# Performance work log

Hardware: AMD Instinct MI355X
Metric: run time of the kernel (lower is better)

## Reference

```python
import math
import jax, jax.numpy as jnp
import numpy as np

D_MODEL = 4096
N_HEADS = 32
N_KV_HEADS = 8
D_HEAD = D_MODEL // N_HEADS  # 128
GROUP = N_HEADS // N_KV_HEADS  # 4
ROPE = dict(rope_theta=500000.0, factor=32.0, hi_freq_factor=4.0, lo_freq_factor=1.0, original_context_length=8192)


def setup_inputs() -> dict:
    key = jax.random.key(0)
    ks = jax.random.split(key, 5)
    B, T = 1, 2048
    s = 0.02
    return {
        "resid": jax.random.normal(ks[0], (B, T, D_MODEL), jnp.float32),
        "Wq": jax.random.normal(ks[1], (D_MODEL, D_MODEL), jnp.float32) * s,
        "Wk": jax.random.normal(ks[2], (D_MODEL, N_KV_HEADS * D_HEAD), jnp.float32) * s,
        "Wv": jax.random.normal(ks[3], (D_MODEL, N_KV_HEADS * D_HEAD), jnp.float32) * s,
        "Wo": jax.random.normal(ks[4], (D_MODEL, D_MODEL), jnp.float32) * s,
    }


def _rope_cos_sin(head_dim, pos, dtype):
    # Llama3 scaled RoPE frequencies
    idx = jnp.arange(0, head_dim, 2, dtype=jnp.float32) / head_dim
    freq = (1.0 / (2.0 * math.pi)) * ROPE["rope_theta"] ** (-idx)
    factor, lo, hi = ROPE["factor"], ROPE["lo_freq_factor"], ROPE["hi_freq_factor"]
    L0 = ROPE["original_context_length"]
    freq_low, freq_high = lo / L0, hi / L0
    freq_scaled = jnp.where(freq < freq_low, freq / factor, freq)
    smooth = jnp.clip((L0 * freq - lo) / (hi - lo), 0.0, 1.0)
    freq_smooth = (1.0 - smooth) * (freq / factor) + smooth * freq
    is_mid = (freq >= freq_low) & (freq <= freq_high)
    freq = jnp.where(is_mid, freq_smooth, freq_scaled)
    phase = 2.0 * math.pi * pos.astype(jnp.float32)[:, None] * freq[None, :]  # [T, dh/2]
    emb = jnp.concatenate([phase, phase], axis=-1)  # [T, dh]
    return jnp.cos(emb).astype(dtype), jnp.sin(emb).astype(dtype)


def _rotate_half(x):
    h = x.shape[-1] // 2
    return jnp.concatenate([-x[..., h:], x[..., :h]], axis=-1)


def reference(resid, Wq, Wk, Wv, Wo):
    B, T, _ = resid.shape
    # projections + head split -> [B, H, T, dh]
    q = (resid @ Wq).reshape(B, T, N_HEADS, D_HEAD).transpose(0, 2, 1, 3)
    k = (resid @ Wk).reshape(B, T, N_KV_HEADS, D_HEAD).transpose(0, 2, 1, 3)
    v = (resid @ Wv).reshape(B, T, N_KV_HEADS, D_HEAD).transpose(0, 2, 1, 3)
    cos, sin = _rope_cos_sin(D_HEAD, jnp.arange(T), resid.dtype)  # [T, dh]
    cos = cos[None, None]  # broadcast over batch and heads
    sin = sin[None, None]
    q = q * cos + _rotate_half(q) * sin
    k = k * cos + _rotate_half(k) * sin
    # GQA scores in fp32: [B, Hkv, G, Tq, Tk]
    qg = q.reshape(B, N_KV_HEADS, GROUP, T, D_HEAD)
    att = jnp.einsum("bhgqd,bhkd->bhgqk", qg.astype(jnp.float32), k.astype(jnp.float32)) / math.sqrt(D_HEAD)
    causal = jnp.tril(jnp.ones((T, T), dtype=bool))  # k <= q
    att = jnp.where(causal[None, None, None], att, -jnp.inf)
    probs = jax.nn.softmax(att, axis=-1).astype(resid.dtype)
    ctx = jnp.einsum("bhgqk,bhkd->bhgqd", probs, v)  # [B, Hkv, G, T, dh]
    out = ctx.reshape(B, N_HEADS, T, D_HEAD).transpose(0, 2, 1, 3).reshape(B, T, D_MODEL)
    return out @ Wo
```

## Files before the change

kernel.cpp:

```cpp
#include <hip/hip_runtime.h>
#include <stdint.h>

#define T_SEQ 2048
#define DMODEL 4096
#define DQKV 6144
#define KOFF 4096
#define VOFF 5120
#define DHEAD 128
#define NHEADS 32
#define NKV 8

typedef unsigned short u16;
typedef __attribute__((ext_vector_type(8))) __bf16 bf16x8;
typedef __attribute__((ext_vector_type(4))) float f32x4;

__device__ __forceinline__ u16 f2bf(float f) {
    uint32_t u = __builtin_bit_cast(uint32_t, f);
    u += 0x7FFFu + ((u >> 16) & 1u);
    return (u16)(u >> 16);
}
__device__ __forceinline__ float bf2f(u16 b) {
    return __builtin_bit_cast(float, (uint32_t)b << 16);
}

__device__ __forceinline__ void gload_lds16(const u16* g, u16* l) {
    __builtin_amdgcn_global_load_lds((const __attribute__((address_space(1))) uint32_t*)g,
                                     (__attribute__((address_space(3))) uint32_t*)l, 16, 0, 0);
}

__global__ void cvt_kernel(const float* __restrict__ in, u16* __restrict__ out, int n4) {
    int i = blockIdx.x * blockDim.x + threadIdx.x;
    int stride = gridDim.x * blockDim.x;
    for (; i < n4; i += stride) {
        float4 v = ((const float4*)in)[i];
        ushort4 o;
        o.x = f2bf(v.x); o.y = f2bf(v.y); o.z = f2bf(v.z); o.w = f2bf(v.w);
        ((ushort4*)out)[i] = o;
    }
}

__global__ void tcvt_kernel(const float* __restrict__ in, u16* __restrict__ out, int R, int C) {
    __shared__ float tile[32][33];
    int c0 = blockIdx.x * 32, r0 = blockIdx.y * 32;
    int tx = threadIdx.x, ty = threadIdx.y;
#pragma unroll
    for (int i = 0; i < 32; i += 8)
        tile[ty + i][tx] = in[(size_t)(r0 + ty + i) * C + c0 + tx];
    __syncthreads();
#pragma unroll
    for (int i = 0; i < 32; i += 8)
        out[(size_t)(c0 + ty + i) * R + r0 + tx] = f2bf(tile[tx][ty + i]);
}

__global__ void vtrans_kernel(const u16* __restrict__ QKV, u16* __restrict__ Vt) {
    __shared__ u16 tile[32][33];
    int t0 = blockIdx.x * 32, d0 = blockIdx.y * 32;
    int tx = threadIdx.x, ty = threadIdx.y;
#pragma unroll
    for (int i = 0; i < 32; i += 8)
        tile[ty + i][tx] = QKV[(size_t)(t0 + ty + i) * DQKV + VOFF + d0 + tx];
    __syncthreads();
#pragma unroll
    for (int i = 0; i < 32; i += 8)
        Vt[(size_t)(d0 + ty + i) * T_SEQ + t0 + tx] = tile[tx][ty + i];
}

__global__ void rope_setup(float* __restrict__ cosT, float* __restrict__ sinT) {
    int t = blockIdx.x, d = threadIdx.x;
    const float TWO_PI = 6.283185307179586f;
    float fidx = (float)d * (1.0f / 64.0f);
    float freq = (1.0f / TWO_PI) * powf(500000.0f, -fidx);
    const float factor = 32.0f, lo = 1.0f, hi = 4.0f, L0 = 8192.0f;
    float fl = lo / L0, fh = hi / L0;
    float smooth = fminf(fmaxf((L0 * freq - lo) / (hi - lo), 0.0f), 1.0f);
    float fs = (1.0f - smooth) * (freq / factor) + smooth * freq;
    float fr = (freq < fl) ? (freq / factor) : freq;
    if (freq >= fl && freq <= fh) fr = fs;
    float ang = TWO_PI * (float)t * fr;
    cosT[t * 64 + d] = cosf(ang);
    sinT[t * 64 + d] = sinf(ang);
}

__global__ void rope_apply(u16* __restrict__ x, const float* __restrict__ cosT,
                           const float* __restrict__ sinT, int nheads, int rowstride, int coloff) {
    int i = blockIdx.x * blockDim.x + threadIdx.x;
    int total = T_SEQ * nheads * 64;
    if (i >= total) return;
    int d = i & 63;
    int h = (i >> 6) % nheads;
    int t = i / (nheads * 64);
    size_t base = (size_t)t * rowstride + coloff + h * 128 + d;
    float x0 = bf2f(x[base]), x1 = bf2f(x[base + 64]);
    float c = cosT[t * 64 + d], s = sinT[t * 64 + d];
    x[base] = f2bf(x0 * c - x1 * s);
    x[base + 64] = f2bf(x1 * c + x0 * s);
}

__launch_bounds__(256, 2)
__global__ void gemm_bt(const u16* __restrict__ A, const u16* __restrict__ Bt,
                        void* __restrict__ Cout, int M, int N, int K, int f32out) {
    __shared__ u16 As[128][64];
    __shared__ u16 Bs[128][64];
    int m0 = blockIdx.y * 128, n0 = blockIdx.x * 128;
    int tid = threadIdx.x;
    int wave = tid >> 6, lane = tid & 63;
    int l15 = lane & 15, lg = lane >> 4;
    int wm = (wave >> 1) * 64, wn = (wave & 1) * 64;
    f32x4 acc[4][4] = {};
    int rowb = tid >> 3, ch = (tid & 7) * 8;
    const u16* Ag = A + (size_t)(m0 + rowb) * K + ch;
    const u16* Bg = Bt + (size_t)(n0 + rowb) * K + ch;
    u16* Al = &As[rowb][ch];
    u16* Bl = &Bs[rowb][ch];

    for (int k0 = 0; k0 < K; k0 += 64) {
        __syncthreads();
#pragma unroll
        for (int p = 0; p < 4; ++p) {
            gload_lds16(Ag + (size_t)(p * 32) * K + k0, Al + p * 32 * 64);
            gload_lds16(Bg + (size_t)(p * 32) * K + k0, Bl + p * 32 * 64);
        }
        __syncthreads();
#pragma unroll
        for (int kk = 0; kk < 64; kk += 32) {
            bf16x8 af[4], bfr[4];
#pragma unroll
            for (int mi = 0; mi < 4; ++mi)
                af[mi] = *(const bf16x8*)&As[wm + mi * 16 + l15][kk + lg * 8];
#pragma unroll
            for (int ni = 0; ni < 4; ++ni)
                bfr[ni] = *(const bf16x8*)&Bs[wn + ni * 16 + l15][kk + lg * 8];
#pragma unroll
            for (int mi = 0; mi < 4; ++mi)
#pragma unroll
                for (int ni = 0; ni < 4; ++ni)
                    acc[mi][ni] = __builtin_amdgcn_mfma_f32_16x16x32_bf16(af[mi], bfr[ni], acc[mi][ni], 0, 0, 0);
        }
    }
#pragma unroll
    for (int mi = 0; mi < 4; ++mi)
#pragma unroll
        for (int ni = 0; ni < 4; ++ni)
#pragma unroll
            for (int r = 0; r < 4; ++r) {
                int row = m0 + wm + mi * 16 + lg * 4 + r;
                int col = n0 + wn + ni * 16 + l15;
                float v = acc[mi][ni][r];
                if (f32out)
                    ((float*)Cout)[(size_t)row * N + col] = v;
                else
                    ((u16*)Cout)[(size_t)row * N + col] = f2bf(v);
            }
}

__launch_bounds__(256, 2)
__global__ void attn_kernel(const u16* __restrict__ QKV, const u16* __restrict__ Vt,
                            u16* __restrict__ ctx) {
    __shared__ u16 Ks[2][64][128];
    __shared__ u16 Vs[2][128][64];
    __shared__ u16 Ones[16][64];
    __shared__ u16 Ps[4][16][72];
    int h = blockIdx.x;
    int q0 = ((int)gridDim.y - 1 - (int)blockIdx.y) * 64;
    int kvh = h >> 2;
    int tid = threadIdx.x;
    int lane = tid & 63;
    int wave = tid >> 6;
    int l15 = lane & 15, lg = lane >> 4;
    int qrow_base = q0 + wave * 16;

    {
        int idx = tid * 4;
        u16 val = (idx < 64) ? (u16)0x3F80 : (u16)0;
        u16* p = &Ones[0][0] + idx;
        p[0] = val; p[1] = val; p[2] = val; p[3] = val;
    }

    bf16x8 qf[4];
#pragma unroll
    for (int kk = 0; kk < 4; ++kk)
        qf[kk] = *(const bf16x8*)&QKV[(size_t)(qrow_base + l15) * DQKV + h * DHEAD + kk * 32 + lg * 8];

    int krow = tid >> 4, kj = tid & 15;
    int vrow = tid >> 3, vj = tid & 7;
    const u16* Kg = QKV + (size_t)krow * DQKV + KOFF + kvh * DHEAD + ((kj ^ krow) * 8);
    const u16* Vg = Vt + (size_t)(kvh * DHEAD + vrow) * T_SEQ + ((vj ^ (vrow & 7)) * 8);
    u16* Kl = &Ks[0][0][0] + tid * 8;
    u16* Vl = &Vs[0][0][0] + tid * 8;
    const int BUFK = 64 * 128;
    const int BUFV = 128 * 64;

#define STAGE(buf, kv0)                                                              \
    {                                                                                \
        _Pragma("unroll")                                                            \
        for (int p = 0; p < 4; ++p) {                                                \
            gload_lds16(Kg + (size_t)((kv0) + p * 16) * DQKV, Kl + (buf) * BUFK + p * 2048); \
            gload_lds16(Vg + (kv0) + (size_t)(p * 32) * T_SEQ, Vl + (buf) * BUFV + p * 2048); \
        }                                                                            \
    }

    f32x4 acc_o[8] = {};
    f32x4 acc_l = {0.f, 0.f, 0.f, 0.f};
    float m_run[4];
#pragma unroll
    for (int r = 0; r < 4; ++r) m_run[r] = -1e30f;

    int ntiles = (q0 >> 6) + 1;
    STAGE(0, 0);

    for (int t = 0; t < ntiles; ++t) {
        int cur = t & 1;
        __syncthreads();
        if (t + 1 < ntiles) STAGE(cur ^ 1, (t + 1) * 64);

        const u16* ksb = &Ks[cur][0][0];
        const u16* vsb = &Vs[cur][0][0];
        int kv0 = t * 64;

        f32x4 sacc[4] = {};
#pragma unroll
        for (int nt = 0; nt < 4; ++nt)
#pragma unroll
            for (int kk = 0; kk < 4; ++kk) {
                int row = nt * 16 + l15;
                int slot = (kk * 4 + lg) ^ l15;
                bf16x8 kf = *(const bf16x8*)(ksb + row * 128 + slot * 8);
                sacc[nt] = __builtin_amdgcn_mfma_f32_16x16x32_bf16(qf[kk], kf, sacc[nt], 0, 0, 0);
            }

        const float scale = 0.08838834764831845f;
        bool diag = (t == ntiles - 1);
#pragma unroll
        for (int r = 0; r < 4; ++r) {
            int qrow = qrow_base + lg * 4 + r;
            float sv[4];
            float pmax = -1e30f;
#pragma unroll
            for (int nt = 0; nt < 4; ++nt) {
                float s = sacc[nt][r] * scale;
                if (diag && (kv0 + nt * 16 + l15 > qrow)) s = -1e30f;
                sv[nt] = s;
                pmax = fmaxf(pmax, s);
            }
#pragma unroll
            for (int m = 1; m < 16; m <<= 1) pmax = fmaxf(pmax, __shfl_xor(pmax, m, 64));
            if (__any(pmax > m_run[r] + 8.0f)) {
                float mnew = fmaxf(m_run[r], pmax);
                float alpha = __expf(m_run[r] - mnew);
                m_run[r] = mnew;
#pragma unroll
                for (int dt = 0; dt < 8; ++dt) acc_o[dt][r] *= alpha;
                acc_l[r] *= alpha;
            }
#pragma unroll
            for (int nt = 0; nt < 4; ++nt)
                Ps[wave][lg * 4 + r][nt * 16 + l15] = f2bf(__expf(sv[nt] - m_run[r]));
        }

        bf16x8 pf[2];
#pragma unroll
        for (int kt = 0; kt < 2; ++kt)
            pf[kt] = *(const bf16x8*)&Ps[wave][l15][kt * 32 + lg * 8];
#pragma unroll
        for (int kt = 0; kt < 2; ++kt) {
            int oslot = (kt * 4 + lg) ^ (l15 & 7);
            bf16x8 of = *(const bf16x8*)(&Ones[0][0] + l15 * 64 + oslot * 8);
            acc_l = __builtin_amdgcn_mfma_f32_16x16x32_bf16(pf[kt], of, acc_l, 0, 0, 0);
        }
#pragma unroll
        for (int dt = 0; dt < 8; ++dt)
#pragma unroll
            for (int kt = 0; kt < 2; ++kt) {
                int vr = dt * 16 + l15;
                int slot = (kt * 4 + lg) ^ (l15 & 7);
                bf16x8 vf = *(const bf16x8*)(vsb + vr * 64 + slot * 8);
                acc_o[dt] = __builtin_amdgcn_mfma_f32_16x16x32_bf16(pf[kt], vf, acc_o[dt], 0, 0, 0);
            }
    }
#undef STAGE

#pragma unroll
    for (int r = 0; r < 4; ++r) {
        float lsum = __shfl(acc_l[r], lg * 16, 64);
        float inv = 1.0f / lsum;
#pragma unroll
        for (int dt = 0; dt < 8; ++dt) {
            int row = qrow_base + lg * 4 + r;
            int col = h * DHEAD + dt * 16 + l15;
            ctx[(size_t)row * DMODEL + col] = f2bf(acc_o[dt][r] * inv);
        }
    }
}

extern "C" void kernel_launch(void* const* d_in, const int* in_sizes, int n_in,
                              void* d_out, int out_size, void* d_ws, size_t ws_size,
                              hipStream_t stream) {
    const float* resid = (const float*)d_in[0];
    const float* Wq = (const float*)d_in[1];
    const float* Wk = (const float*)d_in[2];
    const float* Wv = (const float*)d_in[3];
    const float* Wo = (const float*)d_in[4];

    char* ws = (char*)d_ws;
    u16* Xb   = (u16*)(ws + 0);
    u16* ctx  = (u16*)(ws + 0);
    u16* WqT  = (u16*)(ws + 16777216);
    u16* WkT  = (u16*)(ws + 50331648);
    u16* WvT  = (u16*)(ws + 58720256);
    u16* WoT  = (u16*)(ws + 67108864);
    u16* QKV  = (u16*)(ws + 100663296);
    u16* Vt   = (u16*)(ws + 125829120);
    float* cosT = (float*)(ws + 130023424);
    float* sinT = (float*)(ws + 130547712);

    cvt_kernel<<<2048, 256, 0, stream>>>(resid, Xb, T_SEQ * DMODEL / 4);
    dim3 tb(32, 8);
    tcvt_kernel<<<dim3(DMODEL / 32, DMODEL / 32), tb, 0, stream>>>(Wq, WqT, DMODEL, DMODEL);
    tcvt_kernel<<<dim3(1024 / 32, DMODEL / 32), tb, 0, stream>>>(Wk, WkT, DMODEL, 1024);
    tcvt_kernel<<<dim3(1024 / 32, DMODEL / 32), tb, 0, stream>>>(Wv, WvT, DMODEL, 1024);
    tcvt_kernel<<<dim3(DMODEL / 32, DMODEL / 32), tb, 0, stream>>>(Wo, WoT, DMODEL, DMODEL);
    rope_setup<<<T_SEQ, 64, 0, stream>>>(cosT, sinT);

    gemm_bt<<<dim3(DQKV / 128, T_SEQ / 128), 256, 0, stream>>>(Xb, WqT, QKV, T_SEQ, DQKV, DMODEL, 0);

    rope_apply<<<(T_SEQ * NHEADS * 64 + 255) / 256, 256, 0, stream>>>(QKV, cosT, sinT, NHEADS, DQKV, 0);
    rope_apply<<<(T_SEQ * NKV * 64 + 255) / 256, 256, 0, stream>>>(QKV, cosT, sinT, NKV, DQKV, KOFF);

    vtrans_kernel<<<dim3(T_SEQ / 32, 1024 / 32), tb, 0, stream>>>(QKV, Vt);

    attn_kernel<<<dim3(NHEADS, T_SEQ / 64), 256, 0, stream>>>(QKV, Vt, ctx);

    gemm_bt<<<dim3(DMODEL / 128, T_SEQ / 128), 256, 0, stream>>>(ctx, WoT, d_out, T_SEQ, DMODEL, DMODEL, 1);
}
```

Measured before the change: 377.5 us.

## Retile QKV GEMM to 128x96 and split-K the output projection with atomics

The QKV projection now uses 128x96 tiles, which gives 64x16=1024 workgroups instead of 768 and should fill the CUs better. It also adds an XCD-aware block swizzle. The output projection is split along K into two halves that accumulate into a pre-zeroed fp32 output with atomic adds, which doubles the workgroup count from 512 to 1024. Occupancy hints rise to 4 blocks per CU. The cost is an extra zeroing pass, atomic traffic, and an fp32 summation order that is no longer deterministic.

```diff
diff --git a/kernel.cpp b/kernel.cpp
--- a/kernel.cpp
+++ b/kernel.cpp
@@ -26,6 +26,13 @@
 __device__ __forceinline__ void gload_lds16(const u16* g, u16* l) {
     __builtin_amdgcn_global_load_lds((const __attribute__((address_space(1))) uint32_t*)g,
                                      (__attribute__((address_space(3))) uint32_t*)l, 16, 0, 0);
+}
+
+__global__ void zero_f32(float* __restrict__ p, int n4) {
+    int i = blockIdx.x * blockDim.x + threadIdx.x;
+    int stride = gridDim.x * blockDim.x;
+    float4 z = {0.f, 0.f, 0.f, 0.f};
+    for (; i < n4; i += stride) ((float4*)p)[i] = z;
 }
 
 __global__ void cvt_kernel(const float* __restrict__ in, u16* __restrict__ out, int n4) {
@@ -96,24 +103,90 @@
     x[base + 64] = f2bf(x1 * c + x0 * s);
 }
 
-__launch_bounds__(256, 2)
-__global__ void gemm_bt(const u16* __restrict__ A, const u16* __restrict__ Bt,
-                        void* __restrict__ Cout, int M, int N, int K, int f32out) {
+__launch_bounds__(256, 4)
+__global__ void gemm_bt96(const u16* __restrict__ A, const u16* __restrict__ Bt,
+                          u16* __restrict__ Cout, int M, int N, int K) {
+    __shared__ u16 As[128][64];
+    __shared__ u16 Bs[96][64];
+    int gx = gridDim.x, nwg = gx * gridDim.y;
+    int lin = blockIdx.y * gx + blockIdx.x;
+    int cpx = nwg >> 3;
+    int swz = (lin & 7) * cpx + (lin >> 3);
+    int bx = swz % gx, by = swz / gx;
+    int m0 = by * 128, n0 = bx * 96;
+    int tid = threadIdx.x;
+    int wave = tid >> 6, lane = tid & 63;
+    int l15 = lane & 15, lg = lane >> 4;
+    int wm = (wave >> 1) * 64, wn = (wave & 1) * 48;
+    f32x4 acc[4][3] = {};
+    int rowb = tid >> 3, ch = (tid & 7) * 8;
+    const u16* Ag = A + (size_t)(m0 + rowb) * K + ch;
+    const u16* Bg = Bt + (size_t)(n0 + rowb) * K + ch;
+    u16* Al = &As[rowb][ch];
+    u16* Bl = &Bs[0][0] + tid * 8;
+
+    for (int k0 = 0; k0 < K; k0 += 64) {
+        __syncthreads();
+#pragma unroll
+        for (int p = 0; p < 4; ++p)
+            gload_lds16(Ag + (size_t)(p * 32) * K + k0, Al + p * 32 * 64);
+#pragma unroll
+        for (int p = 0; p < 3; ++p)
+            gload_lds16(Bg + (size_t)(p * 32) * K + k0, Bl + p * 32 * 64);
+        __syncthreads();
+#pragma unroll
+        for (int kk = 0; kk < 64; kk += 32) {
+            bf16x8 af[4], bfr[3];
+#pragma unroll
+            for (int mi = 0; mi < 4; ++mi)
+                af[mi] = *(const bf16x8*)&As[wm + mi * 16 + l15][kk + lg * 8];
+#pragma unroll
+            for (int ni = 0; ni < 3; ++ni)
+                bfr[ni] = *(const bf16x8*)&Bs[wn + ni * 16 + l15][kk + lg * 8];
+#pragma unroll
+            for (int mi = 0; mi < 4; ++mi)
+#pragma unroll
+                for (int ni = 0; ni < 3; ++ni)
+                    acc[mi][ni] = __builtin_amdgcn_mfma_f32_16x16x32_bf16(af[mi], bfr[ni], acc[mi][ni], 0, 0, 0);
+        }
+    }
+#pragma unroll
+    for (int mi = 0; mi < 4; ++mi)
+#pragma unroll
+        for (int ni = 0; ni < 3; ++ni)
+#pragma unroll
+            for (int r = 0; r < 4; ++r) {
+                int row = m0 + wm + mi * 16 + lg * 4 + r;
+                int col = n0 + wn + ni * 16 + l15;
+                Cout[(size_t)row * N + col] = f2bf(acc[mi][ni][r]);
+            }
+}
+
+__launch_bounds__(256, 4)
+__global__ void gemm_bt_splitk(const u16* __restrict__ A, const u16* __restrict__ Bt,
+                               float* __restrict__ Cout, int M, int N, int K, int ksplit) {
     __shared__ u16 As[128][64];
     __shared__ u16 Bs[128][64];
-    int m0 = blockIdx.y * 128, n0 = blockIdx.x * 128;
+    int gx = gridDim.x, nwg = gx * gridDim.y;
+    int lin = blockIdx.y * gx + blockIdx.x;
+    int cpx = nwg >> 3;
+    int swz = (lin & 7) * cpx + (lin >> 3);
+    int bx = swz % gx, by = swz / gx;
+    int m0 = by * 128, n0 = bx * 128;
+    int klen = K / ksplit;
+    int kbase = blockIdx.z * klen;
     int tid = threadIdx.x;
     int wave = tid >> 6, lane = tid & 63;
     int l15 = lane & 15, lg = lane >> 4;
     int wm = (wave >> 1) * 64, wn = (wave & 1) * 64;
     f32x4 acc[4][4] = {};
     int rowb = tid >> 3, ch = (tid & 7) * 8;
-    const u16* Ag = A + (size_t)(m0 + rowb) * K + ch;
-    const u16* Bg = Bt + (size_t)(n0 + rowb) * K + ch;
+    const u16* Ag = A + (size_t)(m0 + rowb) * K + kbase + ch;
+    const u16* Bg = Bt + (size_t)(n0 + rowb) * K + kbase + ch;
     u16* Al = &As[rowb][ch];
     u16* Bl = &Bs[rowb][ch];
 
-    for (int k0 = 0; k0 < K; k0 += 64) {
+    for (int k0 = 0; k0 < klen; k0 += 64) {
         __syncthreads();
 #pragma unroll
         for (int p = 0; p < 4; ++p) {
@@ -145,11 +218,7 @@
             for (int r = 0; r < 4; ++r) {
                 int row = m0 + wm + mi * 16 + lg * 4 + r;
                 int col = n0 + wn + ni * 16 + l15;
-                float v = acc[mi][ni][r];
-                if (f32out)
-                    ((float*)Cout)[(size_t)row * N + col] = v;
-                else
-                    ((u16*)Cout)[(size_t)row * N + col] = f2bf(v);
+                unsafeAtomicAdd(&Cout[(size_t)row * N + col], acc[mi][ni][r]);
             }
 }
 
@@ -321,7 +390,7 @@
     tcvt_kernel<<<dim3(DMODEL / 32, DMODEL / 32), tb, 0, stream>>>(Wo, WoT, DMODEL, DMODEL);
     rope_setup<<<T_SEQ, 64, 0, stream>>>(cosT, sinT);
 
-    gemm_bt<<<dim3(DQKV / 128, T_SEQ / 128), 256, 0, stream>>>(Xb, WqT, QKV, T_SEQ, DQKV, DMODEL, 0);
+    gemm_bt96<<<dim3(DQKV / 96, T_SEQ / 128), 256, 0, stream>>>(Xb, WqT, QKV, T_SEQ, DQKV, DMODEL);
 
     rope_apply<<<(T_SEQ * NHEADS * 64 + 255) / 256, 256, 0, stream>>>(QKV, cosT, sinT, NHEADS, DQKV, 0);
     rope_apply<<<(T_SEQ * NKV * 64 + 255) / 256, 256, 0, stream>>>(QKV, cosT, sinT, NKV, DQKV, KOFF);
@@ -330,5 +399,7 @@
 
     attn_kernel<<<dim3(NHEADS, T_SEQ / 64), 256, 0, stream>>>(QKV, Vt, ctx);
 
-    gemm_bt<<<dim3(DMODEL / 128, T_SEQ / 128), 256, 0, stream>>>(ctx, WoT, d_out, T_SEQ, DMODEL, DMODEL, 1);
-}
+    zero_f32<<<1024, 256, 0, stream>>>((float*)d_out, T_SEQ * DMODEL / 4);
+    gemm_bt_splitk<<<dim3(DMODEL / 128, T_SEQ / 128, 2), 256, 0, stream>>>(
+        ctx, WoT, (float*)d_out, T_SEQ, DMODEL, DMODEL, 2);
+}
```

Result: slower. 417.2 us (+10.5%).

## Replace GEMM with 256x256-tile 8-wave ping-pong pipelined kernel with swizzled LDS

Applied to the files above, without the earlier changes.

Swaps the simple 128x128 single-buffered GEMM for a 512-thread kernel that computes 256x256 tiles. It double-buffers 128 KB of dynamic LDS, interleaves staged global-to-LDS loads with MFMA quarter-phases under explicit barriers and setprio, and XOR-swizzles LDS addresses to avoid bank conflicts. The goal is to overlap memory traffic with matrix math and raise data reuse for both projection GEMMs. The attention kernel's launch bounds are also raised to 3 blocks per CU. The large tiles cut the block count (192 and 128 blocks), which may underfill the 256 CUs, and the 131072-byte LDS request must be allowed at launch.

```diff
diff --git a/kernel.cpp b/kernel.cpp
--- a/kernel.cpp
+++ b/kernel.cpp
@@ -96,64 +96,120 @@
     x[base + 64] = f2bf(x1 * c + x0 * s);
 }
 
-__launch_bounds__(256, 2)
-__global__ void gemm_bt(const u16* __restrict__ A, const u16* __restrict__ Bt,
-                        void* __restrict__ Cout, int M, int N, int K, int f32out) {
-    __shared__ u16 As[128][64];
-    __shared__ u16 Bs[128][64];
-    int m0 = blockIdx.y * 128, n0 = blockIdx.x * 128;
+__launch_bounds__(512, 2)
+__global__ void gemm8p(const u16* __restrict__ A, const u16* __restrict__ Bt,
+                       void* __restrict__ Cout, int M, int N, int K, int f32out) {
+    extern __shared__ u16 lds[];
+    const int TILE = 256 * 64;
+    u16* LA = lds;
+    u16* LB = lds + 2 * TILE;
     int tid = threadIdx.x;
-    int wave = tid >> 6, lane = tid & 63;
+    int lane = tid & 63, wid = tid >> 6;
     int l15 = lane & 15, lg = lane >> 4;
-    int wm = (wave >> 1) * 64, wn = (wave & 1) * 64;
-    f32x4 acc[4][4] = {};
-    int rowb = tid >> 3, ch = (tid & 7) * 8;
-    const u16* Ag = A + (size_t)(m0 + rowb) * K + ch;
-    const u16* Bg = Bt + (size_t)(n0 + rowb) * K + ch;
-    u16* Al = &As[rowb][ch];
-    u16* Bl = &Bs[rowb][ch];
-
-    for (int k0 = 0; k0 < K; k0 += 64) {
-        __syncthreads();
-#pragma unroll
-        for (int p = 0; p < 4; ++p) {
-            gload_lds16(Ag + (size_t)(p * 32) * K + k0, Al + p * 32 * 64);
-            gload_lds16(Bg + (size_t)(p * 32) * K + k0, Bl + p * 32 * 64);
+    int wmL = (wid >> 2) * 128, wnL = (wid & 3) * 64;
+    int m0 = blockIdx.y * 256, n0 = blockIdx.x * 256;
+    int xorv = ((l15 >> 2) & 1) << 4;
+    int rl = tid >> 3, cc = tid & 7;
+    int scc = cc ^ (((rl >> 2) & 1) << 1);
+    const u16* Ag = A + (size_t)(m0 + rl) * K + scc * 8;
+    const u16* Bg = Bt + (size_t)(n0 + rl) * K + scc * 8;
+    int niters = K >> 7;
+
+    f32x4 acc[8][4] = {};
+    bf16x8 a[4][2], b[2][2];
+
+#define STG_A(buf, t, half) { \
+    gload_lds16(Ag + (size_t)((half) * 128) * K + (t) * 64,      LA + (buf) * TILE + ((half) * 128) * 64 + tid * 8);      \
+    gload_lds16(Ag + (size_t)((half) * 128 + 64) * K + (t) * 64, LA + (buf) * TILE + ((half) * 128 + 64) * 64 + tid * 8); }
+#define STG_B(buf, t, half) { \
+    gload_lds16(Bg + (size_t)((half) * 128) * K + (t) * 64,      LB + (buf) * TILE + ((half) * 128) * 64 + tid * 8);      \
+    gload_lds16(Bg + (size_t)((half) * 128 + 64) * K + (t) * 64, LB + (buf) * TILE + ((half) * 128 + 64) * 64 + tid * 8); }
+#define RD_A(buf, qm) { _Pragma("unroll") for (int mi = 0; mi < 4; ++mi) { \
+    int row = wmL + (qm) * 64 + mi * 16 + l15; \
+    a[mi][0] = *(const bf16x8*)&LA[(buf) * TILE + ((row * 64 + lg * 8) ^ xorv)]; \
+    a[mi][1] = *(const bf16x8*)&LA[(buf) * TILE + ((row * 64 + 32 + lg * 8) ^ xorv)]; } }
+#define RD_B(buf, qn) { _Pragma("unroll") for (int ni = 0; ni < 2; ++ni) { \
+    int row = wnL + (qn) * 32 + ni * 16 + l15; \
+    b[ni][0] = *(const bf16x8*)&LB[(buf) * TILE + ((row * 64 + lg * 8) ^ xorv)]; \
+    b[ni][1] = *(const bf16x8*)&LB[(buf) * TILE + ((row * 64 + 32 + lg * 8) ^ xorv)]; } }
+#define MMQ(qm, qn) { _Pragma("unroll") for (int mi = 0; mi < 4; ++mi) \
+    _Pragma("unroll") for (int ni = 0; ni < 2; ++ni) { \
+    acc[(qm)*4+mi][(qn)*2+ni] = __builtin_amdgcn_mfma_f32_16x16x32_bf16(a[mi][0], b[ni][0], acc[(qm)*4+mi][(qn)*2+ni], 0, 0, 0); \
+    acc[(qm)*4+mi][(qn)*2+ni] = __builtin_amdgcn_mfma_f32_16x16x32_bf16(a[mi][1], b[ni][1], acc[(qm)*4+mi][(qn)*2+ni], 0, 0, 0); } }
+#define PH_MID  __builtin_amdgcn_s_barrier(); \
+                asm volatile("s_waitcnt lgkmcnt(0)" ::: "memory"); \
+                __builtin_amdgcn_sched_barrier(0); \
+                __builtin_amdgcn_s_setprio(1)
+#define PH_END  __builtin_amdgcn_s_setprio(0); __builtin_amdgcn_s_barrier()
+
+    STG_A(0, 0, 0); STG_A(0, 0, 1); STG_B(0, 0, 0); STG_B(0, 0, 1);
+    STG_A(1, 1, 0);
+    asm volatile("s_waitcnt vmcnt(2)" ::: "memory");
+    __builtin_amdgcn_sched_barrier(0);
+    __builtin_amdgcn_s_barrier();
+
+    for (int it = 0; it < niters; ++it) {
+        int t0 = 2 * it, t1 = t0 + 1;
+        bool last = (it == niters - 1);
+        RD_A(0, 0); RD_B(0, 0);
+        STG_A(1, t1, 1);
+        PH_MID; MMQ(0, 0); PH_END;
+        RD_B(0, 1);
+        STG_B(1, t1, 0);
+        PH_MID; MMQ(0, 1); PH_END;
+        RD_A(0, 1);
+        STG_B(1, t1, 1);
+        PH_MID; MMQ(1, 1); PH_END;
+        RD_B(0, 0);
+        if (!last) STG_A(0, t0 + 2, 0);
+        PH_MID; MMQ(1, 0);
+        __builtin_amdgcn_s_setprio(0);
+        if (last) { asm volatile("s_waitcnt vmcnt(0)" ::: "memory"); }
+        else      { asm volatile("s_waitcnt vmcnt(2)" ::: "memory"); }
+        __builtin_amdgcn_sched_barrier(0);
+        __builtin_amdgcn_s_barrier();
+        RD_A(1, 0); RD_B(1, 0);
+        if (!last) STG_A(0, t0 + 2, 1);
+        PH_MID; MMQ(0, 0); PH_END;
+        RD_B(1, 1);
+        if (!last) STG_B(0, t0 + 2, 0);
+        PH_MID; MMQ(0, 1); PH_END;
+        RD_A(1, 1);
+        if (!last) STG_B(0, t0 + 2, 1);
+        PH_MID; MMQ(1, 1); PH_END;
+        RD_B(1, 0);
+        if (!last) STG_A(1, t1 + 2, 0);
+        PH_MID; MMQ(1, 0);
+        __builtin_amdgcn_s_setprio(0);
+        if (!last) {
+            asm volatile("s_waitcnt vmcnt(2)" ::: "memory");
+            __builtin_amdgcn_sched_barrier(0);
+            __builtin_amdgcn_s_barrier();
         }
-        __syncthreads();
-#pragma unroll
-        for (int kk = 0; kk < 64; kk += 32) {
-            bf16x8 af[4], bfr[4];
-#pragma unroll
-            for (int mi = 0; mi < 4; ++mi)
-                af[mi] = *(const bf16x8*)&As[wm + mi * 16 + l15][kk + lg * 8];
-#pragma unroll
-            for (int ni = 0; ni < 4; ++ni)
-                bfr[ni] = *(const bf16x8*)&Bs[wn + ni * 16 + l15][kk + lg * 8];
-#pragma unroll
-            for (int mi = 0; mi < 4; ++mi)
-#pragma unroll
-                for (int ni = 0; ni < 4; ++ni)
-                    acc[mi][ni] = __builtin_amdgcn_mfma_f32_16x16x32_bf16(af[mi], bfr[ni], acc[mi][ni], 0, 0, 0);
-        }
-    }
-#pragma unroll
-    for (int mi = 0; mi < 4; ++mi)
-#pragma unroll
-        for (int ni = 0; ni < 4; ++ni)
+    }
+#undef STG_A
+#undef STG_B
+#undef RD_A
+#undef RD_B
+#undef MMQ
+#undef PH_MID
+#undef PH_END
+
+#pragma unroll
+    for (int mi8 = 0; mi8 < 8; ++mi8)
+#pragma unroll
+        for (int ni4 = 0; ni4 < 4; ++ni4)
 #pragma unroll
             for (int r = 0; r < 4; ++r) {
-                int row = m0 + wm + mi * 16 + lg * 4 + r;
-                int col = n0 + wn + ni * 16 + l15;
-                float v = acc[mi][ni][r];
-                if (f32out)
-                    ((float*)Cout)[(size_t)row * N + col] = v;
-                else
-                    ((u16*)Cout)[(size_t)row * N + col] = f2bf(v);
-            }
-}
-
-__launch_bounds__(256, 2)
+                int row = m0 + wmL + (mi8 >> 2) * 64 + (mi8 & 3) * 16 + lg * 4 + r;
+                int col = n0 + wnL + (ni4 >> 1) * 32 + (ni4 & 1) * 16 + l15;
+                float v = acc[mi8][ni4][r];
+                if (f32out) ((float*)Cout)[(size_t)row * N + col] = v;
+                else        ((u16*)Cout)[(size_t)row * N + col] = f2bf(v);
+            }
+}
+
+__launch_bounds__(256, 3)
 __global__ void attn_kernel(const u16* __restrict__ QKV, const u16* __restrict__ Vt,
                             u16* __restrict__ ctx) {
     __shared__ u16 Ks[2][64][128];
@@ -321,7 +377,7 @@
     tcvt_kernel<<<dim3(DMODEL / 32, DMODEL / 32), tb, 0, stream>>>(Wo, WoT, DMODEL, DMODEL);
     rope_setup<<<T_SEQ, 64, 0, stream>>>(cosT, sinT);
 
-    gemm_bt<<<dim3(DQKV / 128, T_SEQ / 128), 256, 0, stream>>>(Xb, WqT, QKV, T_SEQ, DQKV, DMODEL, 0);
+    gemm8p<<<dim3(DQKV / 256, T_SEQ / 256), 512, 131072, stream>>>(Xb, WqT, QKV, T_SEQ, DQKV, DMODEL, 0);
 
     rope_apply<<<(T_SEQ * NHEADS * 64 + 255) / 256, 256, 0, stream>>>(QKV, cosT, sinT, NHEADS, DQKV, 0);
     rope_apply<<<(T_SEQ * NKV * 64 + 255) / 256, 256, 0, stream>>>(QKV, cosT, sinT, NKV, DQKV, KOFF);
@@ -330,5 +386,5 @@
 
     attn_kernel<<<dim3(NHEADS, T_SEQ / 64), 256, 0, stream>>>(QKV, Vt, ctx);
 
-    gemm_bt<<<dim3(DMODEL / 128, T_SEQ / 128), 256, 0, stream>>>(ctx, WoT, d_out, T_SEQ, DMODEL, DMODEL, 1);
-}
+    gemm8p<<<dim3(DMODEL / 256, T_SEQ / 256), 512, 131072, stream>>>(ctx, WoT, d_out, T_SEQ, DMODEL, DMODEL, 1);
+}
```

Measured after the change: 405.1 us. 1.07x slower.
